# Kernel optimization log

Measured on AMD Instinct MI355X. Metric: run time of the kernel, lower is better.

The kernel has to match this reference:

```python
import jax, jax.numpy as jnp
import numpy as np

N_NODES = 50000


def _gat_layer(h, e_feat, Ww, Wb, aw, ab, src, dst):
    # h: [N,1,din], e_feat: [E,1,edim]
    hs = h[src]                                   # [E,1,din] gather src
    hd = h[dst]                                   # [E,1,din] gather dst
    # edge attention logit: relu(attn_fc(cat(src,dst)))
    e = jax.nn.relu(jnp.concatenate([hs, hd], axis=-1) @ aw.T + ab)  # [E,1,1]
    # segment softmax over incoming edges of each dst node
    emax = jax.ops.segment_max(e, dst, num_segments=N_NODES)          # [N,1,1]
    ex = jnp.exp(e - emax[dst])
    denom = jax.ops.segment_sum(ex, dst, num_segments=N_NODES)        # [N,1,1]
    alpha = ex / denom[dst]                                           # [E,1,1]
    # weighted scatter-sum of edge messages (m = edge features)
    z = jax.ops.segment_sum(alpha * e_feat, dst, num_segments=N_NODES)  # [N,1,edim]
    # node update: relu(W_apply(cat(h, z)))
    return jax.nn.relu(jnp.concatenate([h, z], axis=-1) @ Ww.T + Wb)    # [N,1,dout]


def setup_inputs() -> dict:
    key = jax.random.key(0)
    ks = jax.random.split(key, 12)
    N, E, D = N_NODES, 640000, 128
    s = 0.05  # weight scale for numerical sanity
    return {
        "nfeats": jax.random.normal(ks[0], (N, 1, D), jnp.float32),
        "efeats": jax.random.normal(ks[1], (E, 1, D), jnp.float32),
        "W_apply_w0": jax.random.normal(ks[2], (D, 2 * D), jnp.float32) * s,
        "W_apply_b0": jax.random.normal(ks[3], (D,), jnp.float32) * s,
        "attn_w0": jax.random.normal(ks[4], (1, 2 * D), jnp.float32) * s,
        "attn_b0": jax.random.normal(ks[5], (1,), jnp.float32) * s,
        "W_apply_w1": jax.random.normal(ks[6], (D, 2 * D), jnp.float32) * s,
        "W_apply_b1": jax.random.normal(ks[7], (D,), jnp.float32) * s,
        "attn_w1": jax.random.normal(ks[8], (1, 2 * D), jnp.float32) * s,
        "attn_b1": jax.random.normal(ks[9], (1,), jnp.float32) * s,
        "src": jax.random.randint(ks[10], (E,), 0, N, jnp.int32),
        "dst": jax.random.randint(ks[11], (E,), 0, N, jnp.int32),
    }


def reference(nfeats, efeats, W_apply_w0, W_apply_b0, attn_w0, attn_b0,
              W_apply_w1, W_apply_b1, attn_w1, attn_b1, src, dst):
    h = _gat_layer(nfeats, efeats, W_apply_w0, W_apply_b0, attn_w0, attn_b0, src, dst)
    # dropout is identity in eval mode
    h = _gat_layer(h, efeats, W_apply_w1, W_apply_b1, attn_w1, attn_b1, src, dst)
    return h.sum(axis=1)  # [N, dout]
```

## Files before the change

### kernel.cpp

```cpp
#include <hip/hip_runtime.h>


__global__ void hist_k(const int* __restrict__ dst, int* __restrict__ counts, int E){
  int e = blockIdx.x*blockDim.x + threadIdx.x;
  if(e<E) atomicAdd(&counts[dst[e]], 1);
}

__global__ __launch_bounds__(1024) void scan1_k(const int* __restrict__ counts, int* __restrict__ excl,
                                                int* __restrict__ partials, int N){
  __shared__ int tmp[1024];
  int tid = threadIdx.x;
  int i = blockIdx.x*1024 + tid;
  int v = (i<N)? counts[i] : 0;
  tmp[tid] = v;
  __syncthreads();
  for(int off=1; off<1024; off<<=1){
    int t = (tid>=off)? tmp[tid-off] : 0;
    __syncthreads();
    tmp[tid] += t;
    __syncthreads();
  }
  if(i<N) excl[i] = tmp[tid] - v;
  if(tid==1023) partials[blockIdx.x] = tmp[tid];
}

__global__ void scan2_k(int* __restrict__ partials, int NB){
  __shared__ int tmp[64];
  int tid = threadIdx.x;
  int v = (tid<NB)? partials[tid] : 0;
  tmp[tid] = v;
  __syncthreads();
  for(int off=1; off<64; off<<=1){
    int t = (tid>=off)? tmp[tid-off] : 0;
    __syncthreads();
    tmp[tid] += t;
    __syncthreads();
  }
  if(tid<NB) partials[tid] = tmp[tid] - v;
}

__global__ __launch_bounds__(1024) void scan3_k(int* __restrict__ row_ptr, const int* __restrict__ partials,
                                                int* __restrict__ cursors, int N, int E){
  int i = blockIdx.x*1024 + threadIdx.x;
  if(i<N){
    int r = row_ptr[i] + partials[blockIdx.x];
    row_ptr[i] = r;
    cursors[i] = r;
  }
  if(i==0) row_ptr[N] = E;
}

__global__ void scatter_k(const int* __restrict__ src, const int* __restrict__ dst, int* __restrict__ cursors,
                          int* __restrict__ eperm, int* __restrict__ esrc, int E){
  int e = blockIdx.x*blockDim.x + threadIdx.x;
  if(e<E){
    int d = dst[e];
    int p = atomicAdd(&cursors[d], 1);
    eperm[p] = e;
    esrc[p] = src[e];
  }
}


__global__ void attn_k(const float* __restrict__ h, const float* __restrict__ aw, const float* __restrict__ ab,
                       float* __restrict__ a_src, float* __restrict__ a_dst, int N){
  int gid = blockIdx.x*blockDim.x + threadIdx.x;
  int n = gid >> 6, lane = gid & 63;
  if(n >= N) return;
  float2 hv = ((const float2*)(h + (size_t)n*128))[lane];
  float2 wa = ((const float2*)aw)[lane];
  float2 wb = ((const float2*)(aw+128))[lane];
  float s = hv.x*wa.x + hv.y*wa.y;
  float t = hv.x*wb.x + hv.y*wb.y;
  #pragma unroll
  for(int off=32; off>0; off>>=1){
    s += __shfl_xor(s, off, 64);
    t += __shfl_xor(t, off, 64);
  }
  if(lane==0){ a_src[n] = s; a_dst[n] = t + ab[0]; }
}

__global__ __launch_bounds__(256) void agg_k(const float* __restrict__ efeats,
    const float* __restrict__ a_src, const float* __restrict__ a_dst,
    const int* __restrict__ row_ptr, const int* __restrict__ eperm, const int* __restrict__ esrc,
    float* __restrict__ z, int N){
  int gid = blockIdx.x*blockDim.x + threadIdx.x;
  int n = __builtin_amdgcn_readfirstlane(gid >> 6);
  int lane = threadIdx.x & 63;
  if(n >= N) return;
  int beg = __builtin_amdgcn_readfirstlane(row_ptr[n]);
  int end = __builtin_amdgcn_readfirstlane(row_ptr[n+1]);
  float2 acc; acc.x = 0.f; acc.y = 0.f;
  if(beg < end){
    float adn = a_dst[n];
    const float2* ef2 = (const float2*)efeats;
    float ssum = 0.f;
    for(int i = beg; i < end; i += 16){
      float p[16]; int r[16];
      #pragma unroll
      for(int j=0;j<16;j++){
        int idx = i + j;
        int cidx = idx < end ? idx : end - 1;
        int sj = esrc[cidx];
        r[j] = eperm[cidx];
        float e = fmaxf(a_src[sj] + adn, 0.f);
        p[j] = (idx < end) ? __expf(e) : 0.f;
      }
      float2 f[16];
      #pragma unroll
      for(int j=0;j<16;j++) f[j] = ef2[(size_t)r[j]*64 + lane];
      #pragma unroll
      for(int j=0;j<16;j++){
        ssum += p[j];
        acc.x = fmaf(p[j], f[j].x, acc.x);
        acc.y = fmaf(p[j], f[j].y, acc.y);
      }
    }
    float inv = 1.f / ssum;
    acc.x *= inv; acc.y *= inv;
  }
  ((float2*)z)[(size_t)n*64 + lane] = acc;
}

__global__ __launch_bounds__(256) void update_k(const float* __restrict__ h, const float* __restrict__ z,
                                                const float* __restrict__ W, const float* __restrict__ bias,
                                                float* __restrict__ out, int N){
  __shared__ float xs[64][36];
  __shared__ float ws[32][132];
  int tid = threadIdx.x;
  int tx = tid & 15;
  int ty = tid >> 4;
  int n0 = blockIdx.x * 64;
  float acc[4][8];
  #pragma unroll
  for(int i=0;i<4;i++)
    #pragma unroll
    for(int j=0;j<8;j++) acc[i][j] = 0.f;

  int lr = tid >> 2;
  int lk = (tid & 3) * 8;
  int wo = tid >> 1;
  int wk = (tid & 1) * 16;

  for(int kb=0; kb<256; kb+=32){
    {
      int node = n0 + lr;
      float4 v0 = make_float4(0.f,0.f,0.f,0.f), v1 = v0;
      if(node < N){
        int kg = kb + lk;
        const float* sp = (kg < 128) ? (h + (size_t)node*128 + kg)
                                     : (z + (size_t)node*128 + (kg-128));
        v0 = ((const float4*)sp)[0];
        v1 = ((const float4*)sp)[1];
      }
      *(float4*)&xs[lr][lk]   = v0;
      *(float4*)&xs[lr][lk+4] = v1;
    }
    {
      const float* wp = W + (size_t)wo*256 + kb + wk;
      float4 a0 = ((const float4*)wp)[0];
      float4 a1 = ((const float4*)wp)[1];
      float4 a2 = ((const float4*)wp)[2];
      float4 a3 = ((const float4*)wp)[3];
      float vals[16] = {a0.x,a0.y,a0.z,a0.w, a1.x,a1.y,a1.z,a1.w,
                        a2.x,a2.y,a2.z,a2.w, a3.x,a3.y,a3.z,a3.w};
      #pragma unroll
      for(int j=0;j<16;j++) ws[wk+j][wo] = vals[j];
    }
    __syncthreads();
    #pragma unroll 8
    for(int k=0;k<32;k++){
      float xv[4];
      #pragma unroll
      for(int i=0;i<4;i++) xv[i] = xs[ty*4+i][k];
      float4 w0 = *(const float4*)&ws[k][tx*8];
      float4 w1 = *(const float4*)&ws[k][tx*8+4];
      float wv[8] = {w0.x,w0.y,w0.z,w0.w, w1.x,w1.y,w1.z,w1.w};
      #pragma unroll
      for(int i=0;i<4;i++)
        #pragma unroll
        for(int j=0;j<8;j++)
          acc[i][j] += xv[i]*wv[j];
    }
    __syncthreads();
  }

  const float4* b4 = (const float4*)bias;
  float4 bb0 = b4[tx*2], bb1 = b4[tx*2+1];
  #pragma unroll
  for(int i=0;i<4;i++){
    int n = n0 + ty*4 + i;
    if(n >= N) continue;
    float4 r0, r1;
    r0.x = fmaxf(acc[i][0]+bb0.x, 0.f);
    r0.y = fmaxf(acc[i][1]+bb0.y, 0.f);
    r0.z = fmaxf(acc[i][2]+bb0.z, 0.f);
    r0.w = fmaxf(acc[i][3]+bb0.w, 0.f);
    r1.x = fmaxf(acc[i][4]+bb1.x, 0.f);
    r1.y = fmaxf(acc[i][5]+bb1.y, 0.f);
    r1.z = fmaxf(acc[i][6]+bb1.z, 0.f);
    r1.w = fmaxf(acc[i][7]+bb1.w, 0.f);
    float4* op = (float4*)(out + (size_t)n*128 + tx*8);
    op[0] = r0; op[1] = r1;
  }
}


extern "C" void kernel_launch(void* const* d_in, const int* in_sizes, int n_in,
                              void* d_out, int out_size, void* d_ws, size_t ws_size,
                              hipStream_t stream){
  const float* nfeats = (const float*)d_in[0];
  const float* efeats = (const float*)d_in[1];
  const float* Ww0 = (const float*)d_in[2];
  const float* Wb0 = (const float*)d_in[3];
  const float* aw0 = (const float*)d_in[4];
  const float* ab0 = (const float*)d_in[5];
  const float* Ww1 = (const float*)d_in[6];
  const float* Wb1 = (const float*)d_in[7];
  const float* aw1 = (const float*)d_in[8];
  const float* ab1 = (const float*)d_in[9];
  const int* src = (const int*)d_in[10];
  const int* dst = (const int*)d_in[11];
  int E = in_sizes[10];
  int N = in_sizes[0] / 128;

  char* base = (char*)d_ws;
  size_t off = 0;
  auto take = [&](size_t bytes) -> char* {
    char* p = base + off;
    off = (off + bytes + 255) & ~(size_t)255;
    return p;
  };
  int*   counts  = (int*)take((size_t)N*4);
  int*   row_ptr = (int*)take((size_t)(N+1)*4);
  int*   cursors = (int*)take((size_t)N*4);
  int*   partials= (int*)take(256);
  int*   eperm   = (int*)take((size_t)E*4);
  int*   esrc    = (int*)take((size_t)E*4);
  float* a_src   = (float*)take((size_t)N*4);
  float* a_dst   = (float*)take((size_t)N*4);
  float* zbuf    = (float*)take((size_t)N*128*4);
  float* h1      = (float*)take((size_t)N*128*4);

  int NB = (N + 1023)/1024;

  hipMemsetAsync(counts, 0, (size_t)N*4, stream);
  hist_k<<<(E+255)/256, 256, 0, stream>>>(dst, counts, E);
  scan1_k<<<NB, 1024, 0, stream>>>(counts, row_ptr, partials, N);
  scan2_k<<<1, 64, 0, stream>>>(partials, NB);
  scan3_k<<<NB, 1024, 0, stream>>>(row_ptr, partials, cursors, N, E);
  scatter_k<<<(E+255)/256, 256, 0, stream>>>(src, dst, cursors, eperm, esrc, E);

  int agrid = (N + 3)/4;
  attn_k<<<agrid, 256, 0, stream>>>(nfeats, aw0, ab0, a_src, a_dst, N);
  agg_k<<<agrid, 256, 0, stream>>>(efeats, a_src, a_dst, row_ptr, eperm, esrc, zbuf, N);
  update_k<<<(N+63)/64, 256, 0, stream>>>(nfeats, zbuf, Ww0, Wb0, h1, N);
  attn_k<<<agrid, 256, 0, stream>>>(h1, aw1, ab1, a_src, a_dst, N);
  agg_k<<<agrid, 256, 0, stream>>>(efeats, a_src, a_dst, row_ptr, eperm, esrc, zbuf, N);
  update_k<<<(N+63)/64, 256, 0, stream>>>(h1, zbuf, Ww1, Wb1, (float*)d_out, N);
}
```

Measured before the change: 776.9 us.

## Pre-permute edge features into dst-sorted bf16 buffer for contiguous aggregation

Adds a permute kernel that writes edge features in destination-sorted order and rounds them to bf16, packing two values per 32-bit word. Both aggregation passes then stream contiguous rows instead of gathering through eperm. This halves the bytes read per aggregation and removes the random gather. In exchange it adds one full read and scattered write pass over the edge features, and it costs bf16 precision on the edge messages.

```diff
diff --git a/kernel.cpp b/kernel.cpp
--- a/kernel.cpp
+++ b/kernel.cpp
@@ -51,14 +51,28 @@
 }
 
 __global__ void scatter_k(const int* __restrict__ src, const int* __restrict__ dst, int* __restrict__ cursors,
-                          int* __restrict__ eperm, int* __restrict__ esrc, int E){
+                          int* __restrict__ esrc, int* __restrict__ pos, int E){
   int e = blockIdx.x*blockDim.x + threadIdx.x;
   if(e<E){
     int d = dst[e];
     int p = atomicAdd(&cursors[d], 1);
-    eperm[p] = e;
     esrc[p] = src[e];
-  }
+    pos[e] = p;
+  }
+}
+
+__global__ __launch_bounds__(256) void permute_k(const float* __restrict__ efeats,
+    const int* __restrict__ pos, unsigned* __restrict__ efp, int E){
+  int gid = blockIdx.x*blockDim.x + threadIdx.x;
+  int e = gid >> 6, lane = gid & 63;
+  if(e >= E) return;
+  float2 v = ((const float2*)(efeats + (size_t)e*128))[lane];
+  unsigned ux = __float_as_uint(v.x);
+  unsigned uy = __float_as_uint(v.y);
+  ux = (ux + 0x7FFFu + ((ux >> 16) & 1u)) >> 16;
+  uy = (uy + 0x7FFFu + ((uy >> 16) & 1u)) >> 16;
+  int p = pos[e];
+  efp[(size_t)p*64 + lane] = ux | (uy << 16);
 }
 
 
@@ -80,40 +94,40 @@
   if(lane==0){ a_src[n] = s; a_dst[n] = t + ab[0]; }
 }
 
-__global__ __launch_bounds__(256) void agg_k(const float* __restrict__ efeats,
+__global__ __launch_bounds__(256) void agg_k(const unsigned* __restrict__ efp,
     const float* __restrict__ a_src, const float* __restrict__ a_dst,
-    const int* __restrict__ row_ptr, const int* __restrict__ eperm, const int* __restrict__ esrc,
-    float* __restrict__ z, int N){
+    const int* __restrict__ row_ptr, const int* __restrict__ esrc,
+    float* __restrict__ z, int N, int E){
   int gid = blockIdx.x*blockDim.x + threadIdx.x;
-  int n = __builtin_amdgcn_readfirstlane(gid >> 6);
-  int lane = threadIdx.x & 63;
+  int n = gid >> 6, lane = threadIdx.x & 63;
   if(n >= N) return;
-  int beg = __builtin_amdgcn_readfirstlane(row_ptr[n]);
-  int end = __builtin_amdgcn_readfirstlane(row_ptr[n+1]);
+  int beg = row_ptr[n], end = row_ptr[n+1];
   float2 acc; acc.x = 0.f; acc.y = 0.f;
   if(beg < end){
     float adn = a_dst[n];
-    const float2* ef2 = (const float2*)efeats;
     float ssum = 0.f;
     for(int i = beg; i < end; i += 16){
-      float p[16]; int r[16];
+      unsigned f[16];
+      #pragma unroll
+      for(int j=0;j<16;j++){
+        int idx = i + j; idx = idx < E ? idx : E - 1;
+        f[j] = efp[(size_t)idx*64 + lane];
+      }
+      float p[16];
       #pragma unroll
       for(int j=0;j<16;j++){
         int idx = i + j;
         int cidx = idx < end ? idx : end - 1;
-        int sj = esrc[cidx];
-        r[j] = eperm[cidx];
-        float e = fmaxf(a_src[sj] + adn, 0.f);
+        float e = fmaxf(a_src[esrc[cidx]] + adn, 0.f);
         p[j] = (idx < end) ? __expf(e) : 0.f;
       }
-      float2 f[16];
-      #pragma unroll
-      for(int j=0;j<16;j++) f[j] = ef2[(size_t)r[j]*64 + lane];
       #pragma unroll
       for(int j=0;j<16;j++){
         ssum += p[j];
-        acc.x = fmaf(p[j], f[j].x, acc.x);
-        acc.y = fmaf(p[j], f[j].y, acc.y);
+        float fx = __uint_as_float(f[j] << 16);
+        float fy = __uint_as_float(f[j] & 0xFFFF0000u);
+        acc.x = fmaf(p[j], fx, acc.x);
+        acc.y = fmaf(p[j], fy, acc.y);
       }
     }
     float inv = 1.f / ssum;
@@ -231,16 +245,17 @@
     off = (off + bytes + 255) & ~(size_t)255;
     return p;
   };
-  int*   counts  = (int*)take((size_t)N*4);
-  int*   row_ptr = (int*)take((size_t)(N+1)*4);
-  int*   cursors = (int*)take((size_t)N*4);
-  int*   partials= (int*)take(256);
-  int*   eperm   = (int*)take((size_t)E*4);
-  int*   esrc    = (int*)take((size_t)E*4);
-  float* a_src   = (float*)take((size_t)N*4);
-  float* a_dst   = (float*)take((size_t)N*4);
-  float* zbuf    = (float*)take((size_t)N*128*4);
-  float* h1      = (float*)take((size_t)N*128*4);
+  int*      counts  = (int*)take((size_t)N*4);
+  int*      row_ptr = (int*)take((size_t)(N+1)*4);
+  int*      cursors = (int*)take((size_t)N*4);
+  int*      partials= (int*)take(256);
+  int*      pos     = (int*)take((size_t)E*4);
+  int*      esrc    = (int*)take((size_t)E*4);
+  float*    a_src   = (float*)take((size_t)N*4);
+  float*    a_dst   = (float*)take((size_t)N*4);
+  float*    zbuf    = (float*)take((size_t)N*128*4);
+  float*    h1      = (float*)take((size_t)N*128*4);
+  unsigned* efp     = (unsigned*)take((size_t)E*64*4);
 
   int NB = (N + 1023)/1024;
 
@@ -249,13 +264,14 @@
   scan1_k<<<NB, 1024, 0, stream>>>(counts, row_ptr, partials, N);
   scan2_k<<<1, 64, 0, stream>>>(partials, NB);
   scan3_k<<<NB, 1024, 0, stream>>>(row_ptr, partials, cursors, N, E);
-  scatter_k<<<(E+255)/256, 256, 0, stream>>>(src, dst, cursors, eperm, esrc, E);
+  scatter_k<<<(E+255)/256, 256, 0, stream>>>(src, dst, cursors, esrc, pos, E);
+  permute_k<<<(E+3)/4, 256, 0, stream>>>(efeats, pos, efp, E);
 
   int agrid = (N + 3)/4;
   attn_k<<<agrid, 256, 0, stream>>>(nfeats, aw0, ab0, a_src, a_dst, N);
-  agg_k<<<agrid, 256, 0, stream>>>(efeats, a_src, a_dst, row_ptr, eperm, esrc, zbuf, N);
+  agg_k<<<agrid, 256, 0, stream>>>(efp, a_src, a_dst, row_ptr, esrc, zbuf, N, E);
   update_k<<<(N+63)/64, 256, 0, stream>>>(nfeats, zbuf, Ww0, Wb0, h1, N);
   attn_k<<<agrid, 256, 0, stream>>>(h1, aw1, ab1, a_src, a_dst, N);
-  agg_k<<<agrid, 256, 0, stream>>>(efeats, a_src, a_dst, row_ptr, eperm, esrc, zbuf, N);
+  agg_k<<<agrid, 256, 0, stream>>>(efp, a_src, a_dst, row_ptr, esrc, zbuf, N, E);
   update_k<<<(N+63)/64, 256, 0, stream>>>(h1, zbuf, Ww1, Wb1, (float*)d_out, N);
 }
```

Result: slower. 798.3 us (+2.7%).
